# Kernel optimization log

Hardware: AMD Instinct MI355X
Metric: run time of the kernel (lower is better)

The kernel has to match this reference:

```python
import jax, jax.numpy as jnp
import numpy as np
from jax import lax

D_MODEL = 1024
D_STATE = 16
D_CONV = 4
EXPAND = 2
INNER = EXPAND * D_MODEL


def setup_inputs() -> dict:
    key = jax.random.key(0)
    ks = jax.random.split(key, 8)
    B, L = 2, 1024
    x = jax.random.normal(ks[0], (B, L, D_MODEL), dtype=jnp.float32)
    W_in = jax.random.normal(ks[1], (2 * INNER, D_MODEL), dtype=jnp.float32) * (1.0 / np.sqrt(D_MODEL))
    conv_w = jax.random.normal(ks[2], (INNER, 1, D_CONV), dtype=jnp.float32) * (1.0 / np.sqrt(D_CONV))
    conv_b = jax.random.normal(ks[3], (INNER,), dtype=jnp.float32) * 0.02
    A = jax.random.normal(ks[4], (INNER, D_STATE), dtype=jnp.float32) * 0.1
    B_param = jax.random.normal(ks[5], (INNER, D_STATE), dtype=jnp.float32) * 0.1
    C_param = jax.random.normal(ks[6], (INNER, D_STATE), dtype=jnp.float32) * 0.1
    D_param = jnp.ones((INNER,), dtype=jnp.float32)
    W_out = jax.random.normal(ks[7], (D_MODEL, INNER), dtype=jnp.float32) * (1.0 / np.sqrt(INNER))
    return {"x": x, "W_in": W_in, "conv_w": conv_w, "conv_b": conv_b,
            "A": A, "B_param": B_param, "C_param": C_param, "D_param": D_param,
            "W_out": W_out}


def _mamba_fwd(x, W_in, conv_w, conv_b, A, B_param, C_param, W_out):
    Bsz, L, _ = x.shape
    inner = A.shape[0]
    # in_proj then interleaved split: view (B,L,inner,2) -> x=[...,0], gate=[...,1]
    xp = jnp.einsum('bld,ed->ble', x, W_in).reshape(Bsz, L, inner, 2)
    u, gate = xp[..., 0], xp[..., 1]
    # depthwise causal conv (torch pads both sides d_conv-1 then slices [:L] == left pad only)
    u_ncl = jnp.transpose(u, (0, 2, 1))  # (B, inner, L)
    conv = lax.conv_general_dilated(
        u_ncl, conv_w,
        window_strides=(1,), padding=[(D_CONV - 1, 0)],
        dimension_numbers=('NCH', 'OIH', 'NCH'),
        feature_group_count=inner)
    conv = conv + conv_b[None, :, None]
    xc = jnp.transpose(conv, (0, 2, 1))  # (B, L, inner)
    delta = jax.nn.sigmoid(xc)
    # discretized params, time-major for scan: (L, B, inner, d_state)
    a = jnp.transpose(A[None, None] * delta[..., None], (1, 0, 2, 3))
    bx = jnp.transpose(B_param[None, None] * (delta * xc)[..., None], (1, 0, 2, 3))

    def step(state, inp):
        a_l, bx_l = inp
        state = a_l * state + bx_l                       # (B, inner, d_state)
        y = jnp.einsum('bns,ns->bn', state, C_param)     # (B, inner)
        return state, y

    state0 = jnp.zeros((Bsz, inner, A.shape[1]), dtype=x.dtype)
    _, ys = lax.scan(step, state0, (a, bx))              # ys: (L, B, inner)
    out = jnp.transpose(ys, (1, 0, 2)) * jax.nn.sigmoid(gate)
    return jnp.einsum('bln,dn->bld', out, W_out)


def reference(x, W_in, conv_w, conv_b, A, B_param, C_param, D_param, W_out):
    # D_param is defined by the module but unused in its forward; kept for fidelity.
    return _mamba_fwd(x, W_in, conv_w, conv_b, A, B_param, C_param, W_out)
```

## Files before the change

kernel.cpp:

```cpp
#include <hip/hip_runtime.h>
#include <hip/hip_bf16.h>

#define D_MODEL 1024
#define INNER   2048
#define NPROJ   4096
#define BSZ     2
#define LSEQ    1024
#define MROWS   (BSZ*LSEQ)

#define CHUNK 32
#define WARM  24
#define NCHK  (LSEQ / CHUNK)

using short8   = __attribute__((ext_vector_type(8))) short;
using ushort8  = __attribute__((ext_vector_type(8))) unsigned short;
using f32x4    = __attribute__((ext_vector_type(4))) float;
using i32x4    = __attribute__((ext_vector_type(4))) int;
using char16v  = __attribute__((ext_vector_type(16))) char;
typedef unsigned short ushort;
typedef unsigned char uchar;

#define MFMA16(A,B,Cv) __builtin_amdgcn_mfma_f32_16x16x32_bf16(A,B,Cv,0,0,0)
#define MFMAI8(A,B,Cv) __builtin_amdgcn_mfma_i32_16x16x64_i8(A,B,Cv,0,0,0)

__device__ __forceinline__ ushort tobf(float x) {
    return (ushort)(__builtin_bit_cast(unsigned, x) >> 16);
}
__device__ __forceinline__ float frombf(ushort h) {
    return __builtin_bit_cast(float, ((unsigned)h) << 16);
}
__device__ __forceinline__ void glds16(const void* g, void* l) {
    __builtin_amdgcn_global_load_lds((const __attribute__((address_space(1))) void*)g,
                                     (__attribute__((address_space(3))) void*)l, 16, 0, 0);
}

__global__ __launch_bounds__(256) void quant_rows(
    const float* __restrict__ W, uchar* __restrict__ Wh, uchar* __restrict__ Wl,
    float* __restrict__ sW, int RW,
    const float* __restrict__ X, uchar* __restrict__ Xh, uchar* __restrict__ Xl,
    float* __restrict__ sX)
{
    const int K = 1024, KT64 = K / 64;
    int gw = blockIdx.x * 4 + (threadIdx.x >> 6);
    int lane = threadIdx.x & 63;
    const float* src; uchar *dh, *dl; float* ss; int r;
    if (gw < RW) { r = gw;      src = W + (size_t)r * K; dh = Wh; dl = Wl; ss = sW; }
    else         { r = gw - RW; src = X + (size_t)r * K; dh = Xh; dl = Xl; ss = sX; }

    float v[16];
#pragma unroll
    for (int p = 0; p < 4; ++p) {
        float4 f = *reinterpret_cast<const float4*>(src + lane * 16 + p * 4);
        v[p*4+0] = f.x; v[p*4+1] = f.y; v[p*4+2] = f.z; v[p*4+3] = f.w;
    }
    float mx = 0.f;
#pragma unroll
    for (int j = 0; j < 16; ++j) mx = fmaxf(mx, fabsf(v[j]));
#pragma unroll
    for (int off = 1; off < 64; off <<= 1) mx = fmaxf(mx, __shfl_xor(mx, off));
    float s1 = fmaxf(mx, 1e-20f) / 127.f;
    if (lane == 0) ss[r] = s1;
    float inv = 1.f / s1;
    char16v hb, lb;
#pragma unroll
    for (int j = 0; j < 16; ++j) {
        float t = v[j] * inv;
        float h = rintf(t);
        float l = rintf((t - h) * 256.f);
        l = fminf(fmaxf(l, -128.f), 127.f);
        hb[j] = (char)(int)h;
        lb[j] = (char)(int)l;
    }
    size_t byte = (((size_t)(r >> 4) * KT64 + (lane >> 2)) * 64
                   + ((lane & 3) << 4) + (r & 15)) * 16;
    *reinterpret_cast<i32x4*>(dh + byte) = *reinterpret_cast<const i32x4*>(&hb);
    *reinterpret_cast<i32x4*>(dl + byte) = *reinterpret_cast<const i32x4*>(&lb);
}

__global__ __launch_bounds__(512, 1) void gemm1_i8(
    const uchar* __restrict__ Xh, const uchar* __restrict__ Xl, const float* __restrict__ sX,
    const uchar* __restrict__ Wh, const uchar* __restrict__ Wl, const float* __restrict__ sW,
    float* __restrict__ C)
{
    constexpr int KT64 = D_MODEL / 64;
    constexpr int NT = 16;
    __shared__ uchar Ah[3][8192], Al[3][8192];
    __shared__ uchar Bh[3][16384], Bl[3][16384];

    const int tid = threadIdx.x;
    const int wid = tid >> 6, lane = tid & 63;
    const int lm = lane & 15, lk = lane >> 4;

    constexpr int NTX = NPROJ / 256;
    constexpr int CPX = (NTX * (MROWS / 128)) / 8;
    int lin = blockIdx.y * NTX + blockIdx.x;
    int swz = (lin & 7) * CPX + (lin >> 3);
    const int m0 = (swz / NTX) * 128, n0 = (swz % NTX) * 256;
    const int wm = (wid >> 2) * 64, wn = (wid & 3) * 64;

    i32x4 acc1[4][4] = {};
    i32x4 acc2[4][4] = {};

    auto issueB = [&](const uchar* __restrict__ src, uchar* dst, int t, int ci) {
        int s = wid + ci * 8;
        const uchar* g = src + ((size_t)((n0 >> 4) + s) * KT64 + t) * 1024 + lane * 16;
        glds16(g, dst + s * 1024);
    };
    auto issueA = [&](const uchar* __restrict__ src, uchar* dst, int t) {
        const uchar* g = src + ((size_t)((m0 >> 4) + wid) * KT64 + t) * 1024 + lane * 16;
        glds16(g, dst + wid * 1024);
    };
    auto stageTile = [&](int t, int b) {
        issueB(Wh, &Bh[b][0], t, 0); issueB(Wh, &Bh[b][0], t, 1);
        issueB(Wl, &Bl[b][0], t, 0); issueB(Wl, &Bl[b][0], t, 1);
        issueA(Xh, &Ah[b][0], t);    issueA(Xl, &Al[b][0], t);
    };

    stageTile(0, 0);
    stageTile(1, 1);
    asm volatile("s_waitcnt vmcnt(6)" ::: "memory");
    __builtin_amdgcn_s_barrier();

    i32x4 ah[4], bh[4];
#pragma unroll
    for (int i = 0; i < 4; ++i)
        ah[i] = *reinterpret_cast<const i32x4*>(&Ah[0][((wm >> 4) + i) * 1024 + lane * 16]);
#pragma unroll
    for (int q = 0; q < 4; ++q)
        bh[q] = *reinterpret_cast<const i32x4*>(&Bh[0][((wn >> 4) + q) * 1024 + lane * 16]);

    int cur = 0;
    for (int t = 0; t < NT; ++t) {
        int nxt = cur + 1; if (nxt == 3) nxt = 0;
        int stg = cur + 2; if (stg >= 3) stg -= 3;
        const bool pf = (t + 2 < NT);
        i32x4 bl[4], al[4];

        asm volatile("s_waitcnt lgkmcnt(0)" ::: "memory");
        __builtin_amdgcn_sched_barrier(0);
        __builtin_amdgcn_s_setprio(1);
#pragma unroll
        for (int i = 0; i < 4; ++i)
#pragma unroll
            for (int q = 0; q < 4; ++q)
                acc1[i][q] = MFMAI8(ah[i], bh[q], acc1[i][q]);
        __builtin_amdgcn_s_setprio(0);
#pragma unroll
        for (int q = 0; q < 4; ++q)
            bl[q] = *reinterpret_cast<const i32x4*>(&Bl[cur][((wn >> 4) + q) * 1024 + lane * 16]);
        if (pf) {
            issueB(Wh, &Bh[stg][0], t + 2, 0);
            issueB(Wh, &Bh[stg][0], t + 2, 1);
        }

        asm volatile("s_waitcnt lgkmcnt(0)" ::: "memory");
        __builtin_amdgcn_sched_barrier(0);
        __builtin_amdgcn_s_setprio(1);
#pragma unroll
        for (int i = 0; i < 4; ++i)
#pragma unroll
            for (int q = 0; q < 4; ++q)
                acc2[i][q] = MFMAI8(ah[i], bl[q], acc2[i][q]);
        __builtin_amdgcn_s_setprio(0);
#pragma unroll
        for (int i = 0; i < 4; ++i)
            al[i] = *reinterpret_cast<const i32x4*>(&Al[cur][((wm >> 4) + i) * 1024 + lane * 16]);
        if (pf) {
            issueB(Wl, &Bl[stg][0], t + 2, 0);
            issueB(Wl, &Bl[stg][0], t + 2, 1);
        }
        __builtin_amdgcn_s_barrier();

        asm volatile("s_waitcnt lgkmcnt(0)" ::: "memory");
        __builtin_amdgcn_sched_barrier(0);
        __builtin_amdgcn_s_setprio(1);
#pragma unroll
        for (int i = 0; i < 4; ++i)
#pragma unroll
            for (int q = 0; q < 4; ++q)
                acc2[i][q] = MFMAI8(al[i], bh[q], acc2[i][q]);
        __builtin_amdgcn_s_setprio(0);
        if (pf) {
            issueA(Xh, &Ah[stg][0], t + 2);
            issueA(Xl, &Al[stg][0], t + 2);
        }
        if (pf) asm volatile("s_waitcnt vmcnt(6)" ::: "memory");
        else    asm volatile("s_waitcnt vmcnt(0)" ::: "memory");
        __builtin_amdgcn_s_barrier();

        if (t + 1 < NT) {
#pragma unroll
            for (int i = 0; i < 4; ++i)
                ah[i] = *reinterpret_cast<const i32x4*>(&Ah[nxt][((wm >> 4) + i) * 1024 + lane * 16]);
#pragma unroll
            for (int q = 0; q < 4; ++q)
                bh[q] = *reinterpret_cast<const i32x4*>(&Bh[nxt][((wn >> 4) + q) * 1024 + lane * 16]);
        }
        cur = nxt;
    }

#pragma unroll
    for (int i = 0; i < 4; ++i) {
        int r0 = m0 + wm + i * 16 + lk * 4;
        float4 s4 = *reinterpret_cast<const float4*>(&sX[r0]);
        float sa[4] = {s4.x, s4.y, s4.z, s4.w};
#pragma unroll
        for (int j = 0; j < 4; ++j) {
            int col = n0 + wn + j * 16 + lm;
            float sb = sW[col];
#pragma unroll
            for (int r = 0; r < 4; ++r) {
                float o = sa[r] * sb *
                    ((float)acc1[i][j][r] + (float)acc2[i][j][r] * 0.00390625f);
                C[(size_t)(r0 + r) * NPROJ + col] = o;
            }
        }
    }
}

template<int K>
__device__ __forceinline__ void split_chunk(const float* __restrict__ in,
                                            ushort* __restrict__ hi,
                                            ushort* __restrict__ lo, int c) {
    int l = c & 63, sub = c >> 6;
    constexpr int KT = K / 32;
    int kt = sub % KT, rt = sub / KT;
    const float* src = in + (size_t)(rt * 16 + (l & 15)) * K + kt * 32 + (l >> 4) * 8;
    ushort8 h, lw;
#pragma unroll
    for (int j = 0; j < 8; ++j) {
        float x = src[j];
        h[j]  = tobf(x);
        lw[j] = tobf(x - frombf(h[j]));
    }
    *reinterpret_cast<ushort8*>(&hi[(size_t)c * 8]) = h;
    *reinterpret_cast<ushort8*>(&lo[(size_t)c * 8]) = lw;
}

template<int K>
__global__ __launch_bounds__(256) void splitbf_frag(const float* __restrict__ in,
                                                    ushort* __restrict__ hi,
                                                    ushort* __restrict__ lo, int nchunks) {
    int c = blockIdx.x * 256 + threadIdx.x;
    if (c >= nchunks) return;
    split_chunk<K>(in, hi, lo, c);
}

template<int BN, int NCOL, int K, int SPLITK, bool PARTIAL, int NBUF, int NTHR>
__global__ __launch_bounds__(NTHR, 1) void gemm_pipe(
    const ushort* __restrict__ Agh, const ushort* __restrict__ Agl,
    const ushort* __restrict__ Bgh, const ushort* __restrict__ Bgl,
    float* __restrict__ C0, float* __restrict__ Crest)
{
    constexpr int BM = 128;
    constexpr int NW = NTHR / 64;
    constexpr int KT = K / 32;
    constexpr int NT = KT / SPLITK;
    constexpr int CB = (BN / 16) / NW;
    constexpr int CA = (BM / 16) / NW;
    __shared__ ushort Ah[NBUF][BM * 32], Al[NBUF][BM * 32];
    __shared__ ushort Bh[NBUF][BN * 32], Bl[NBUF][BN * 32];

    const int tid = threadIdx.x;
    const int wid = tid >> 6, lane = tid & 63;
    const int lm = lane & 15, lk = lane >> 4;

    constexpr int NTX = NCOL / BN;
    constexpr int NXY = NTX * (MROWS / BM);
    constexpr int CPX = NXY / 8;
    int lin = blockIdx.y * NTX + blockIdx.x;
    int swz = (lin & 7) * CPX + (lin >> 3);
    const int m0 = (swz / NTX) * BM, n0 = (swz % NTX) * BN;
    const int t0 = (SPLITK > 1 ? blockIdx.z : 0) * NT;
    const int wm = (NW == 8) ? (wid >> 2) * 64 : (wid >> 1) * 64;
    const int wn = (NW == 8) ? (wid & 3) * 64 : (wid & 1) * 64;

    f32x4 acc[4][4] = {};

    auto issueB = [&](const ushort* __restrict__ src, ushort* dst, int tg) {
#pragma unroll
        for (int ci = 0; ci < CB; ++ci) {
            int s = wid + ci * NW;
            const ushort* g = src + ((size_t)((n0 >> 4) + s) * KT + tg) * 512 + lane * 8;
            glds16(g, dst + s * 512);
        }
    };
    auto issueA = [&](const ushort* __restrict__ src, ushort* dst, int tg) {
#pragma unroll
        for (int ci = 0; ci < CA; ++ci) {
            int s = wid + ci * NW;
            const ushort* g = src + ((size_t)((m0 >> 4) + s) * KT + tg) * 512 + lane * 8;
            glds16(g, dst + s * 512);
        }
    };
    auto stageTile = [&](int t, int b) {
        issueB(Bgh, &Bh[b][0], t0 + t);
        issueB(Bgl, &Bl[b][0], t0 + t);
        issueA(Agh, &Ah[b][0], t0 + t);
        issueA(Agl, &Al[b][0], t0 + t);
    };

    if constexpr (NBUF == 3) {
        stageTile(0, 0);
        stageTile(1, 1);
        asm volatile("s_waitcnt vmcnt(6)" ::: "memory");
    } else {
        stageTile(0, 0);
        asm volatile("s_waitcnt vmcnt(0)" ::: "memory");
    }
    __builtin_amdgcn_s_barrier();

    short8 ah[4], bh[4];
#pragma unroll
    for (int i = 0; i < 4; ++i)
        ah[i] = *reinterpret_cast<const short8*>(&Ah[0][((wm >> 4) + i) * 512 + lane * 8]);
#pragma unroll
    for (int q = 0; q < 4; ++q)
        bh[q] = *reinterpret_cast<const short8*>(&Bh[0][((wn >> 4) + q) * 512 + lane * 8]);

    int cur = 0;
    for (int t = 0; t < NT; ++t) {
        int nxt, stg;
        bool pf;
        if constexpr (NBUF == 3) {
            nxt = cur + 1; if (nxt == 3) nxt = 0;
            stg = cur + 2; if (stg >= 3) stg -= 3;
            pf = (t + 2 < NT);
        } else {
            nxt = cur ^ 1;
            stg = nxt;
            pf = (t + 1 < NT);
        }
        const int tpre = (NBUF == 3) ? t + 2 : t + 1;
        short8 bl[4], al[4];

        asm volatile("s_waitcnt lgkmcnt(0)" ::: "memory");
        __builtin_amdgcn_sched_barrier(0);
        __builtin_amdgcn_s_setprio(1);
#pragma unroll
        for (int i = 0; i < 4; ++i)
#pragma unroll
            for (int q = 0; q < 4; ++q)
                acc[i][q] = MFMA16(ah[i], bh[q], acc[i][q]);
        __builtin_amdgcn_s_setprio(0);
#pragma unroll
        for (int q = 0; q < 4; ++q)
            bl[q] = *reinterpret_cast<const short8*>(&Bl[cur][((wn >> 4) + q) * 512 + lane * 8]);
        if (pf) issueB(Bgh, &Bh[stg][0], t0 + tpre);

        asm volatile("s_waitcnt lgkmcnt(0)" ::: "memory");
        __builtin_amdgcn_sched_barrier(0);
        __builtin_amdgcn_s_setprio(1);
#pragma unroll
        for (int i = 0; i < 4; ++i)
#pragma unroll
            for (int q = 0; q < 4; ++q)
                acc[i][q] = MFMA16(ah[i], bl[q], acc[i][q]);
        __builtin_amdgcn_s_setprio(0);
#pragma unroll
        for (int i = 0; i < 4; ++i)
            al[i] = *reinterpret_cast<const short8*>(&Al[cur][((wm >> 4) + i) * 512 + lane * 8]);
        if (pf) issueB(Bgl, &Bl[stg][0], t0 + tpre);
        __builtin_amdgcn_s_barrier();

        asm volatile("s_waitcnt lgkmcnt(0)" ::: "memory");
        __builtin_amdgcn_sched_barrier(0);
        __builtin_amdgcn_s_setprio(1);
#pragma unroll
        for (int i = 0; i < 4; ++i)
#pragma unroll
            for (int q = 0; q < 4; ++q)
                acc[i][q] = MFMA16(al[i], bh[q], acc[i][q]);
        __builtin_amdgcn_s_setprio(0);
        if (pf) {
            issueA(Agh, &Ah[stg][0], t0 + tpre);
            issueA(Agl, &Al[stg][0], t0 + tpre);
        }
        if (NBUF == 3 && pf) asm volatile("s_waitcnt vmcnt(6)" ::: "memory");
        else                 asm volatile("s_waitcnt vmcnt(0)" ::: "memory");
        __builtin_amdgcn_s_barrier();

        if (t + 1 < NT) {
#pragma unroll
            for (int i = 0; i < 4; ++i)
                ah[i] = *reinterpret_cast<const short8*>(&Ah[nxt][((wm >> 4) + i) * 512 + lane * 8]);
#pragma unroll
            for (int q = 0; q < 4; ++q)
                bh[q] = *reinterpret_cast<const short8*>(&Bh[nxt][((wn >> 4) + q) * 512 + lane * 8]);
        }
        cur = nxt;
    }

    float* C = C0;
    if constexpr (PARTIAL) {
        int kz = blockIdx.z;
        if (kz != 0) C = Crest + (size_t)(kz - 1) * MROWS * NCOL;
    }
#pragma unroll
    for (int i = 0; i < 4; ++i)
#pragma unroll
        for (int j = 0; j < 4; ++j)
#pragma unroll
            for (int r = 0; r < 4; ++r) {
                int row = m0 + wm + i * 16 + lk * 4 + r;
                int col = n0 + wn + j * 16 + lm;
                C[(size_t)row * NCOL + col] = acc[i][j][r];
            }
}

__global__ __launch_bounds__(256) void reduce_sk(float* __restrict__ out,
                                                 const float* __restrict__ rest) {
    constexpr size_t MN = (size_t)MROWS * D_MODEL;
    size_t i = ((size_t)blockIdx.x * 256 + threadIdx.x) * 4;
    f32x4 a = *reinterpret_cast<const f32x4*>(&out[i]);
    f32x4 b = *reinterpret_cast<const f32x4*>(&rest[i]);
    f32x4 c = *reinterpret_cast<const f32x4*>(&rest[MN + i]);
    f32x4 d = *reinterpret_cast<const f32x4*>(&rest[2 * MN + i]);
    *reinterpret_cast<f32x4*>(&out[i]) = (a + b) + (c + d);
}

__global__ __launch_bounds__(256) void scan_kernel(
    const float* __restrict__ xp,
    const float* __restrict__ conv_w, const float* __restrict__ conv_b,
    const float* __restrict__ Aa, const float* __restrict__ Bp, const float* __restrict__ Cp,
    ushort* __restrict__ yhi, ushort* __restrict__ ylo)
{
    const int NB = INNER / 256;
    int tid = threadIdx.x;
    int bi = blockIdx.x;
    int b  = bi / (NCHK * NB);
    int r  = bi % (NCHK * NB);
    int ch = r / NB;
    int n  = (r % NB) * 256 + tid;

    float4 w = *reinterpret_cast<const float4*>(&conv_w[n * 4]);
    float cb = conv_b[n];
    float An[16], Bn[16], Cn[16], st[16];
#pragma unroll
    for (int i = 0; i < 16; i += 4) {
        float4 va = *reinterpret_cast<const float4*>(&Aa[n * 16 + i]);
        float4 vb = *reinterpret_cast<const float4*>(&Bp[n * 16 + i]);
        float4 vc = *reinterpret_cast<const float4*>(&Cp[n * 16 + i]);
        An[i]=va.x; An[i+1]=va.y; An[i+2]=va.z; An[i+3]=va.w;
        Bn[i]=vb.x; Bn[i+1]=vb.y; Bn[i+2]=vb.z; Bn[i+3]=vb.w;
        Cn[i]=vc.x; Cn[i+1]=vc.y; Cn[i+2]=vc.z; Cn[i+3]=vc.w;
    }
#pragma unroll
    for (int s = 0; s < 16; ++s) st[s] = 0.f;

    int out0 = ch * CHUNK;
    int lstart = (out0 >= WARM) ? (out0 - WARM) : 0;
    float u0 = 0.f, u1 = 0.f, u2 = 0.f;
    const float* xb = xp + (size_t)b * LSEQ * NPROJ;
    size_t fcol = (size_t)(n >> 5) * 512 + ((n >> 3) & 3) * 128 + (n & 7);

    for (int l = lstart; l < out0; l += 8) {
        float uv[8];
#pragma unroll
        for (int i = 0; i < 8; ++i)
            uv[i] = xb[(size_t)(l + i) * NPROJ + 2 * n];
#pragma unroll
        for (int i = 0; i < 8; ++i) {
            float ul = uv[i];
            float xc = cb + w.x * u0 + w.y * u1 + w.z * u2 + w.w * ul;
            u0 = u1; u1 = u2; u2 = ul;
            float d = 1.f / (1.f + __expf(-xc));
            float dxc = d * xc;
#pragma unroll
            for (int s = 0; s < 16; ++s)
                st[s] = (An[s] * d) * st[s] + Bn[s] * dxc;
        }
    }
    for (int lt = 0; lt < CHUNK; lt += 8) {
        float uv[8], gv[8];
#pragma unroll
        for (int i = 0; i < 8; ++i) {
            float2 ug = *reinterpret_cast<const float2*>(
                &xb[(size_t)(out0 + lt + i) * NPROJ + 2 * n]);
            uv[i] = ug.x; gv[i] = ug.y;
        }
#pragma unroll
        for (int i = 0; i < 8; ++i) {
            float ul = uv[i];
            float xc = cb + w.x * u0 + w.y * u1 + w.z * u2 + w.w * ul;
            u0 = u1; u1 = u2; u2 = ul;
            float d = 1.f / (1.f + __expf(-xc));
            float dxc = d * xc;
            float y0 = 0.f, y1 = 0.f, y2 = 0.f, y3 = 0.f;
#pragma unroll
            for (int s = 0; s < 16; s += 4) {
                st[s + 0] = (An[s + 0] * d) * st[s + 0] + Bn[s + 0] * dxc;
                st[s + 1] = (An[s + 1] * d) * st[s + 1] + Bn[s + 1] * dxc;
                st[s + 2] = (An[s + 2] * d) * st[s + 2] + Bn[s + 2] * dxc;
                st[s + 3] = (An[s + 3] * d) * st[s + 3] + Bn[s + 3] * dxc;
                y0 += st[s + 0] * Cn[s + 0];
                y1 += st[s + 1] * Cn[s + 1];
                y2 += st[s + 2] * Cn[s + 2];
                y3 += st[s + 3] * Cn[s + 3];
            }
            float y = (y0 + y1) + (y2 + y3);
            float g = 1.f / (1.f + __expf(-gv[i]));
            float o = y * g;
            int R = b * LSEQ + out0 + lt + i;
            size_t fi = ((size_t)(R >> 4) * 64) * 512 + fcol + (R & 15) * 8;
            ushort hh = tobf(o);
            yhi[fi] = hh;
            ylo[fi] = tobf(o - frombf(hh));
        }
    }
}

extern "C" void kernel_launch(void* const* d_in, const int* in_sizes, int n_in,
                              void* d_out, int out_size, void* d_ws, size_t ws_size,
                              hipStream_t stream) {
    const float* x      = (const float*)d_in[0];
    const float* W_in   = (const float*)d_in[1];
    const float* conv_w = (const float*)d_in[2];
    const float* conv_b = (const float*)d_in[3];
    const float* A      = (const float*)d_in[4];
    const float* Bp     = (const float*)d_in[5];
    const float* Cp     = (const float*)d_in[6];
    const float* W_out  = (const float*)d_in[8];
    float* out = (float*)d_out;

    char* ws = (char*)d_ws;
    float* xp    = (float*)ws;
    uchar* Wh8   = (uchar*)(ws + (32u << 20));
    uchar* Wl8   = (uchar*)(ws + (36u << 20));
    float* sW    = (float*)(ws + (40u << 20));
    ushort* yghi = (ushort*)(ws + (32u << 20));
    ushort* yglo = (ushort*)(ws + (40u << 20));
    ushort* Wohi = (ushort*)ws;
    ushort* Wolo = (ushort*)(ws + (4u << 20));
    float*  Prest = (float*)(ws + (8u << 20));
    uchar* xh8 = (uchar*)d_out;
    uchar* xl8 = xh8 + (2u << 20);
    float* sX  = (float*)(xh8 + (4u << 20));

    dim3 blk(256);
    quant_rows<<<dim3((NPROJ + MROWS) / 4), blk, 0, stream>>>(
        W_in, Wh8, Wl8, sW, NPROJ, x, xh8, xl8, sX);
    gemm1_i8<<<dim3(16, 16), dim3(512), 0, stream>>>(
        xh8, xl8, sX, Wh8, Wl8, sW, xp);
    scan_kernel<<<dim3(BSZ * NCHK * (INNER / 256)), blk, 0, stream>>>(
        xp, conv_w, conv_b, A, Bp, Cp, yghi, yglo);
    splitbf_frag<INNER><<<dim3((D_MODEL * INNER / 8) / 256), blk, 0, stream>>>(
        W_out, Wohi, Wolo, D_MODEL * INNER / 8);
    gemm_pipe<128, D_MODEL, INNER, 4, true, 2, 256>
        <<<dim3(8, 16, 4), dim3(256), 0, stream>>>(yghi, yglo, Wohi, Wolo, out, Prest);
    reduce_sk<<<dim3((MROWS * D_MODEL / 4) / 256), blk, 0, stream>>>(out, Prest);
}
```

Baseline: 104.7 us.

## Switch output projection GEMM from split-bf16 to int8 hi/lo quantized MFMA

The output projection GEMM now uses the same int8 hi/lo per-row-scaled scheme as the input projection, running i8 MFMAs instead of bf16 MFMAs. The goal is to use the higher int8 matrix throughput for the compute-heavy out-proj GEMM. The scan kernel now writes plain fp32 gated outputs, and a generalized quantization kernel (templated on K) quantizes both those activations and W_out. The cost is an extra full fp32 round trip of the 2048x2048 activation buffer through memory. The approximation still depends on the two-level int8 split keeping enough precision.

```diff
diff --git a/kernel.cpp b/kernel.cpp
--- a/kernel.cpp
+++ b/kernel.cpp
@@ -12,69 +12,66 @@
 #define WARM  24
 #define NCHK  (LSEQ / CHUNK)
 
-using short8   = __attribute__((ext_vector_type(8))) short;
-using ushort8  = __attribute__((ext_vector_type(8))) unsigned short;
 using f32x4    = __attribute__((ext_vector_type(4))) float;
 using i32x4    = __attribute__((ext_vector_type(4))) int;
 using char16v  = __attribute__((ext_vector_type(16))) char;
 typedef unsigned short ushort;
 typedef unsigned char uchar;
 
-#define MFMA16(A,B,Cv) __builtin_amdgcn_mfma_f32_16x16x32_bf16(A,B,Cv,0,0,0)
 #define MFMAI8(A,B,Cv) __builtin_amdgcn_mfma_i32_16x16x64_i8(A,B,Cv,0,0,0)
 
-__device__ __forceinline__ ushort tobf(float x) {
-    return (ushort)(__builtin_bit_cast(unsigned, x) >> 16);
-}
-__device__ __forceinline__ float frombf(ushort h) {
-    return __builtin_bit_cast(float, ((unsigned)h) << 16);
-}
 __device__ __forceinline__ void glds16(const void* g, void* l) {
     __builtin_amdgcn_global_load_lds((const __attribute__((address_space(1))) void*)g,
                                      (__attribute__((address_space(3))) void*)l, 16, 0, 0);
 }
 
-__global__ __launch_bounds__(256) void quant_rows(
-    const float* __restrict__ W, uchar* __restrict__ Wh, uchar* __restrict__ Wl,
-    float* __restrict__ sW, int RW,
-    const float* __restrict__ X, uchar* __restrict__ Xh, uchar* __restrict__ Xl,
-    float* __restrict__ sX)
+template<int K>
+__global__ __launch_bounds__(256) void quant2src(
+    const float* __restrict__ S1, uchar* __restrict__ h1, uchar* __restrict__ l1,
+    float* __restrict__ sc1, int R1,
+    const float* __restrict__ S2, uchar* __restrict__ h2, uchar* __restrict__ l2,
+    float* __restrict__ sc2)
 {
-    const int K = 1024, KT64 = K / 64;
+    constexpr int CH = K / 1024;
+    constexpr int KT64 = K / 64;
     int gw = blockIdx.x * 4 + (threadIdx.x >> 6);
     int lane = threadIdx.x & 63;
     const float* src; uchar *dh, *dl; float* ss; int r;
-    if (gw < RW) { r = gw;      src = W + (size_t)r * K; dh = Wh; dl = Wl; ss = sW; }
-    else         { r = gw - RW; src = X + (size_t)r * K; dh = Xh; dl = Xl; ss = sX; }
-
-    float v[16];
-#pragma unroll
-    for (int p = 0; p < 4; ++p) {
-        float4 f = *reinterpret_cast<const float4*>(src + lane * 16 + p * 4);
+    if (gw < R1) { r = gw;      src = S1 + (size_t)r * K; dh = h1; dl = l1; ss = sc1; }
+    else         { r = gw - R1; src = S2 + (size_t)r * K; dh = h2; dl = l2; ss = sc2; }
+
+    float v[16 * CH];
+#pragma unroll
+    for (int p = 0; p < 4 * CH; ++p) {
+        float4 f = *reinterpret_cast<const float4*>(src + lane * 16 * CH + p * 4);
         v[p*4+0] = f.x; v[p*4+1] = f.y; v[p*4+2] = f.z; v[p*4+3] = f.w;
     }
     float mx = 0.f;
 #pragma unroll
-    for (int j = 0; j < 16; ++j) mx = fmaxf(mx, fabsf(v[j]));
+    for (int j = 0; j < 16 * CH; ++j) mx = fmaxf(mx, fabsf(v[j]));
 #pragma unroll
     for (int off = 1; off < 64; off <<= 1) mx = fmaxf(mx, __shfl_xor(mx, off));
     float s1 = fmaxf(mx, 1e-20f) / 127.f;
     if (lane == 0) ss[r] = s1;
     float inv = 1.f / s1;
-    char16v hb, lb;
-#pragma unroll
-    for (int j = 0; j < 16; ++j) {
-        float t = v[j] * inv;
-        float h = rintf(t);
-        float l = rintf((t - h) * 256.f);
-        l = fminf(fmaxf(l, -128.f), 127.f);
-        hb[j] = (char)(int)h;
-        lb[j] = (char)(int)l;
-    }
-    size_t byte = (((size_t)(r >> 4) * KT64 + (lane >> 2)) * 64
-                   + ((lane & 3) << 4) + (r & 15)) * 16;
-    *reinterpret_cast<i32x4*>(dh + byte) = *reinterpret_cast<const i32x4*>(&hb);
-    *reinterpret_cast<i32x4*>(dl + byte) = *reinterpret_cast<const i32x4*>(&lb);
+#pragma unroll
+    for (int c = 0; c < CH; ++c) {
+        char16v hb, lb;
+#pragma unroll
+        for (int j = 0; j < 16; ++j) {
+            float t = v[c * 16 + j] * inv;
+            float h = rintf(t);
+            float l = rintf((t - h) * 256.f);
+            l = fminf(fmaxf(l, -128.f), 127.f);
+            hb[j] = (char)(int)h;
+            lb[j] = (char)(int)l;
+        }
+        int gc = lane * CH + c;
+        size_t byte = (((size_t)(r >> 4) * KT64 + (gc >> 2)) * 64
+                       + ((gc & 3) << 4) + (r & 15)) * 16;
+        *reinterpret_cast<i32x4*>(dh + byte) = *reinterpret_cast<const i32x4*>(&hb);
+        *reinterpret_cast<i32x4*>(dl + byte) = *reinterpret_cast<const i32x4*>(&lb);
+    }
 }
 
 __global__ __launch_bounds__(512, 1) void gemm1_i8(
@@ -218,121 +215,72 @@
     }
 }
 
-template<int K>
-__device__ __forceinline__ void split_chunk(const float* __restrict__ in,
-                                            ushort* __restrict__ hi,
-                                            ushort* __restrict__ lo, int c) {
-    int l = c & 63, sub = c >> 6;
-    constexpr int KT = K / 32;
-    int kt = sub % KT, rt = sub / KT;
-    const float* src = in + (size_t)(rt * 16 + (l & 15)) * K + kt * 32 + (l >> 4) * 8;
-    ushort8 h, lw;
-#pragma unroll
-    for (int j = 0; j < 8; ++j) {
-        float x = src[j];
-        h[j]  = tobf(x);
-        lw[j] = tobf(x - frombf(h[j]));
-    }
-    *reinterpret_cast<ushort8*>(&hi[(size_t)c * 8]) = h;
-    *reinterpret_cast<ushort8*>(&lo[(size_t)c * 8]) = lw;
-}
-
-template<int K>
-__global__ __launch_bounds__(256) void splitbf_frag(const float* __restrict__ in,
-                                                    ushort* __restrict__ hi,
-                                                    ushort* __restrict__ lo, int nchunks) {
-    int c = blockIdx.x * 256 + threadIdx.x;
-    if (c >= nchunks) return;
-    split_chunk<K>(in, hi, lo, c);
-}
-
-template<int BN, int NCOL, int K, int SPLITK, bool PARTIAL, int NBUF, int NTHR>
-__global__ __launch_bounds__(NTHR, 1) void gemm_pipe(
-    const ushort* __restrict__ Agh, const ushort* __restrict__ Agl,
-    const ushort* __restrict__ Bgh, const ushort* __restrict__ Bgl,
+__global__ __launch_bounds__(256, 2) void gemm2_i8(
+    const uchar* __restrict__ Yh, const uchar* __restrict__ Yl, const float* __restrict__ sY,
+    const uchar* __restrict__ Wh, const uchar* __restrict__ Wl, const float* __restrict__ sW,
     float* __restrict__ C0, float* __restrict__ Crest)
 {
-    constexpr int BM = 128;
-    constexpr int NW = NTHR / 64;
-    constexpr int KT = K / 32;
-    constexpr int NT = KT / SPLITK;
-    constexpr int CB = (BN / 16) / NW;
-    constexpr int CA = (BM / 16) / NW;
-    __shared__ ushort Ah[NBUF][BM * 32], Al[NBUF][BM * 32];
-    __shared__ ushort Bh[NBUF][BN * 32], Bl[NBUF][BN * 32];
+    constexpr int KT64 = INNER / 64;
+    constexpr int SPLITK = 4;
+    constexpr int NT = KT64 / SPLITK;
+    __shared__ uchar Ah[2][8192], Al[2][8192];
+    __shared__ uchar Bh[2][8192], Bl[2][8192];
 
     const int tid = threadIdx.x;
     const int wid = tid >> 6, lane = tid & 63;
     const int lm = lane & 15, lk = lane >> 4;
 
-    constexpr int NTX = NCOL / BN;
-    constexpr int NXY = NTX * (MROWS / BM);
-    constexpr int CPX = NXY / 8;
+    constexpr int NTX = D_MODEL / 128;
+    constexpr int CPX = (NTX * (MROWS / 128)) / 8;
     int lin = blockIdx.y * NTX + blockIdx.x;
     int swz = (lin & 7) * CPX + (lin >> 3);
-    const int m0 = (swz / NTX) * BM, n0 = (swz % NTX) * BN;
-    const int t0 = (SPLITK > 1 ? blockIdx.z : 0) * NT;
-    const int wm = (NW == 8) ? (wid >> 2) * 64 : (wid >> 1) * 64;
-    const int wn = (NW == 8) ? (wid & 3) * 64 : (wid & 1) * 64;
-
-    f32x4 acc[4][4] = {};
-
-    auto issueB = [&](const ushort* __restrict__ src, ushort* dst, int tg) {
-#pragma unroll
-        for (int ci = 0; ci < CB; ++ci) {
-            int s = wid + ci * NW;
-            const ushort* g = src + ((size_t)((n0 >> 4) + s) * KT + tg) * 512 + lane * 8;
-            glds16(g, dst + s * 512);
+    const int m0 = (swz / NTX) * 128, n0 = (swz % NTX) * 128;
+    const int t0 = blockIdx.z * NT;
+    const int wm = (wid >> 1) * 64, wn = (wid & 1) * 64;
+
+    i32x4 acc1[4][4] = {};
+    i32x4 acc2[4][4] = {};
+
+    auto issueB = [&](const uchar* __restrict__ src, uchar* dst, int tg) {
+#pragma unroll
+        for (int ci = 0; ci < 2; ++ci) {
+            int s = wid + ci * 4;
+            const uchar* g = src + ((size_t)((n0 >> 4) + s) * KT64 + tg) * 1024 + lane * 16;
+            glds16(g, dst + s * 1024);
         }
     };
-    auto issueA = [&](const ushort* __restrict__ src, ushort* dst, int tg) {
-#pragma unroll
-        for (int ci = 0; ci < CA; ++ci) {
-            int s = wid + ci * NW;
-            const ushort* g = src + ((size_t)((m0 >> 4) + s) * KT + tg) * 512 + lane * 8;
-            glds16(g, dst + s * 512);
+    auto issueA = [&](const uchar* __restrict__ src, uchar* dst, int tg) {
+#pragma unroll
+        for (int ci = 0; ci < 2; ++ci) {
+            int s = wid + ci * 4;
+            const uchar* g = src + ((size_t)((m0 >> 4) + s) * KT64 + tg) * 1024 + lane * 16;
+            glds16(g, dst + s * 1024);
         }
     };
-    auto stageTile = [&](int t, int b) {
-        issueB(Bgh, &Bh[b][0], t0 + t);
-        issueB(Bgl, &Bl[b][0], t0 + t);
-        issueA(Agh, &Ah[b][0], t0 + t);
-        issueA(Agl, &Al[b][0], t0 + t);
+    auto stageTile = [&](int tg, int b) {
+        issueB(Wh, &Bh[b][0], tg);
+        issueB(Wl, &Bl[b][0], tg);
+        issueA(Yh, &Ah[b][0], tg);
+        issueA(Yl, &Al[b][0], tg);
     };
 
-    if constexpr (NBUF == 3) {
-        stageTile(0, 0);
-        stageTile(1, 1);
-        asm volatile("s_waitcnt vmcnt(6)" ::: "memory");
-    } else {
-        stageTile(0, 0);
-        asm volatile("s_waitcnt vmcnt(0)" ::: "memory");
-    }
+    stageTile(t0, 0);
+    asm volatile("s_waitcnt vmcnt(0)" ::: "memory");
     __builtin_amdgcn_s_barrier();
 
-    short8 ah[4], bh[4];
+    i32x4 ah[4], bh[4];
 #pragma unroll
     for (int i = 0; i < 4; ++i)
-        ah[i] = *reinterpret_cast<const short8*>(&Ah[0][((wm >> 4) + i) * 512 + lane * 8]);
+        ah[i] = *reinterpret_cast<const i32x4*>(&Ah[0][((wm >> 4) + i) * 1024 + lane * 16]);
 #pragma unroll
     for (int q = 0; q < 4; ++q)
-        bh[q] = *reinterpret_cast<const short8*>(&Bh[0][((wn >> 4) + q) * 512 + lane * 8]);
+        bh[q] = *reinterpret_cast<const i32x4*>(&Bh[0][((wn >> 4) + q) * 1024 + lane * 16]);
 
     int cur = 0;
     for (int t = 0; t < NT; ++t) {
-        int nxt, stg;
-        bool pf;
-        if constexpr (NBUF == 3) {
-            nxt = cur + 1; if (nxt == 3) nxt = 0;
-            stg = cur + 2; if (stg >= 3) stg -= 3;
-            pf = (t + 2 < NT);
-        } else {
-            nxt = cur ^ 1;
-            stg = nxt;
-            pf = (t + 1 < NT);
-        }
-        const int tpre = (NBUF == 3) ? t + 2 : t + 1;
-        short8 bl[4], al[4];
+        int nxt = cur ^ 1;
+        const bool pf = (t + 1 < NT);
+        i32x4 bl[4], al[4];
 
         asm volatile("s_waitcnt lgkmcnt(0)" ::: "memory");
         __builtin_amdgcn_sched_barrier(0);
@@ -341,12 +289,12 @@
         for (int i = 0; i < 4; ++i)
 #pragma unroll
             for (int q = 0; q < 4; ++q)
-                acc[i][q] = MFMA16(ah[i], bh[q], acc[i][q]);
+                acc1[i][q] = MFMAI8(ah[i], bh[q], acc1[i][q]);
         __builtin_amdgcn_s_setprio(0);
 #pragma unroll
         for (int q = 0; q < 4; ++q)
-            bl[q] = *reinterpret_cast<const short8*>(&Bl[cur][((wn >> 4) + q) * 512 + lane * 8]);
-        if (pf) issueB(Bgh, &Bh[stg][0], t0 + tpre);
+            bl[q] = *reinterpret_cast<const i32x4*>(&Bl[cur][((wn >> 4) + q) * 1024 + lane * 16]);
+        if (pf) issueB(Wh, &Bh[nxt][0], t0 + t + 1);
 
         asm volatile("s_waitcnt lgkmcnt(0)" ::: "memory");
         __builtin_amdgcn_sched_barrier(0);
@@ -355,12 +303,12 @@
         for (int i = 0; i < 4; ++i)
 #pragma unroll
             for (int q = 0; q < 4; ++q)
-                acc[i][q] = MFMA16(ah[i], bl[q], acc[i][q]);
+                acc2[i][q] = MFMAI8(ah[i], bl[q], acc2[i][q]);
         __builtin_amdgcn_s_setprio(0);
 #pragma unroll
         for (int i = 0; i < 4; ++i)
-            al[i] = *reinterpret_cast<const short8*>(&Al[cur][((wm >> 4) + i) * 512 + lane * 8]);
-        if (pf) issueB(Bgl, &Bl[stg][0], t0 + tpre);
+            al[i] = *reinterpret_cast<const i32x4*>(&Al[cur][((wm >> 4) + i) * 1024 + lane * 16]);
+        if (pf) issueB(Wl, &Bl[nxt][0], t0 + t + 1);
         __builtin_amdgcn_s_barrier();
 
         asm volatile("s_waitcnt lgkmcnt(0)" ::: "memory");
@@ -370,42 +318,45 @@
         for (int i = 0; i < 4; ++i)
 #pragma unroll
             for (int q = 0; q < 4; ++q)
-                acc[i][q] = MFMA16(al[i], bh[q], acc[i][q]);
+                acc2[i][q] = MFMAI8(al[i], bh[q], acc2[i][q]);
         __builtin_amdgcn_s_setprio(0);
         if (pf) {
-            issueA(Agh, &Ah[stg][0], t0 + tpre);
-            issueA(Agl, &Al[stg][0], t0 + tpre);
-        }
-        if (NBUF == 3 && pf) asm volatile("s_waitcnt vmcnt(6)" ::: "memory");
-        else                 asm volatile("s_waitcnt vmcnt(0)" ::: "memory");
+            issueA(Yh, &Ah[nxt][0], t0 + t + 1);
+            issueA(Yl, &Al[nxt][0], t0 + t + 1);
+        }
+        asm volatile("s_waitcnt vmcnt(0)" ::: "memory");
         __builtin_amdgcn_s_barrier();
 
         if (t + 1 < NT) {
 #pragma unroll
             for (int i = 0; i < 4; ++i)
-                ah[i] = *reinterpret_cast<const short8*>(&Ah[nxt][((wm >> 4) + i) * 512 + lane * 8]);
-#pragma unroll
-            for (int q = 0; q < 4; ++q)
-                bh[q] = *reinterpret_cast<const short8*>(&Bh[nxt][((wn >> 4) + q) * 512 + lane * 8]);
+                ah[i] = *reinterpret_cast<const i32x4*>(&Ah[nxt][((wm >> 4) + i) * 1024 + lane * 16]);
+#pragma unroll
+            for (int q = 0; q < 4; ++q)
+                bh[q] = *reinterpret_cast<const i32x4*>(&Bh[nxt][((wn >> 4) + q) * 1024 + lane * 16]);
         }
         cur = nxt;
     }
 
-    float* C = C0;
-    if constexpr (PARTIAL) {
-        int kz = blockIdx.z;
-        if (kz != 0) C = Crest + (size_t)(kz - 1) * MROWS * NCOL;
-    }
-#pragma unroll
-    for (int i = 0; i < 4; ++i)
-#pragma unroll
-        for (int j = 0; j < 4; ++j)
+    int kz = blockIdx.z;
+    float* C = (kz == 0) ? C0 : (Crest + (size_t)(kz - 1) * MROWS * D_MODEL);
+#pragma unroll
+    for (int i = 0; i < 4; ++i) {
+        int r0 = m0 + wm + i * 16 + lk * 4;
+        float4 s4 = *reinterpret_cast<const float4*>(&sY[r0]);
+        float sa[4] = {s4.x, s4.y, s4.z, s4.w};
+#pragma unroll
+        for (int j = 0; j < 4; ++j) {
+            int col = n0 + wn + j * 16 + lm;
+            float sb = sW[col];
 #pragma unroll
             for (int r = 0; r < 4; ++r) {
-                int row = m0 + wm + i * 16 + lk * 4 + r;
-                int col = n0 + wn + j * 16 + lm;
-                C[(size_t)row * NCOL + col] = acc[i][j][r];
+                float o = sa[r] * sb *
+                    ((float)acc1[i][j][r] + (float)acc2[i][j][r] * 0.00390625f);
+                C[(size_t)(r0 + r) * D_MODEL + col] = o;
             }
+        }
+    }
 }
 
 __global__ __launch_bounds__(256) void reduce_sk(float* __restrict__ out,
@@ -423,7 +374,7 @@
     const float* __restrict__ xp,
     const float* __restrict__ conv_w, const float* __restrict__ conv_b,
     const float* __restrict__ Aa, const float* __restrict__ Bp, const float* __restrict__ Cp,
-    ushort* __restrict__ yhi, ushort* __restrict__ ylo)
+    float* __restrict__ yg)
 {
     const int NB = INNER / 256;
     int tid = threadIdx.x;
@@ -452,7 +403,6 @@
     int lstart = (out0 >= WARM) ? (out0 - WARM) : 0;
     float u0 = 0.f, u1 = 0.f, u2 = 0.f;
     const float* xb = xp + (size_t)b * LSEQ * NPROJ;
-    size_t fcol = (size_t)(n >> 5) * 512 + ((n >> 3) & 3) * 128 + (n & 7);
 
     for (int l = lstart; l < out0; l += 8) {
         float uv[8];
@@ -500,12 +450,8 @@
             }
             float y = (y0 + y1) + (y2 + y3);
             float g = 1.f / (1.f + __expf(-gv[i]));
-            float o = y * g;
             int R = b * LSEQ + out0 + lt + i;
-            size_t fi = ((size_t)(R >> 4) * 64) * 512 + fcol + (R & 15) * 8;
-            ushort hh = tobf(o);
-            yhi[fi] = hh;
-            ylo[fi] = tobf(o - frombf(hh));
+            yg[(size_t)R * INNER + n] = y * g;
         }
     }
 }
@@ -528,25 +474,28 @@
     uchar* Wh8   = (uchar*)(ws + (32u << 20));
     uchar* Wl8   = (uchar*)(ws + (36u << 20));
     float* sW    = (float*)(ws + (40u << 20));
-    ushort* yghi = (ushort*)(ws + (32u << 20));
-    ushort* yglo = (ushort*)(ws + (40u << 20));
-    ushort* Wohi = (ushort*)ws;
-    ushort* Wolo = (ushort*)(ws + (4u << 20));
-    float*  Prest = (float*)(ws + (8u << 20));
+    float* yg    = (float*)(ws + (32u << 20));
+    uchar* ygh8  = (uchar*)ws;
+    uchar* ygl8  = (uchar*)(ws + (4u << 20));
+    float* Prest = (float*)(ws + (8u << 20));
+    uchar* woh8  = (uchar*)(ws + (48u << 20));
+    uchar* wol8  = (uchar*)(ws + (50u << 20));
+    float* sY    = (float*)(ws + (52u << 20));
+    float* sWo   = (float*)(ws + (52u << 20) + (16u << 10));
     uchar* xh8 = (uchar*)d_out;
     uchar* xl8 = xh8 + (2u << 20);
     float* sX  = (float*)(xh8 + (4u << 20));
 
     dim3 blk(256);
-    quant_rows<<<dim3((NPROJ + MROWS) / 4), blk, 0, stream>>>(
+    quant2src<D_MODEL><<<dim3((NPROJ + MROWS) / 4), blk, 0, stream>>>(
         W_in, Wh8, Wl8, sW, NPROJ, x, xh8, xl8, sX);
     gemm1_i8<<<dim3(16, 16), dim3(512), 0, stream>>>(
         xh8, xl8, sX, Wh8, Wl8, sW, xp);
     scan_kernel<<<dim3(BSZ * NCHK * (INNER / 256)), blk, 0, stream>>>(
-        xp, conv_w, conv_b, A, Bp, Cp, yghi, yglo);
-    splitbf_frag<INNER><<<dim3((D_MODEL * INNER / 8) / 256), blk, 0, stream>>>(
-        W_out, Wohi, Wolo, D_MODEL * INNER / 8);
-    gemm_pipe<128, D_MODEL, INNER, 4, true, 2, 256>
-        <<<dim3(8, 16, 4), dim3(256), 0, stream>>>(yghi, yglo, Wohi, Wolo, out, Prest);
+        xp, conv_w, conv_b, A, Bp, Cp, yg);
+    quant2src<INNER><<<dim3((MROWS + D_MODEL) / 4), blk, 0, stream>>>(
+        yg, ygh8, ygl8, sY, MROWS, W_out, woh8, wol8, sWo);
+    gemm2_i8<<<dim3(8, 16, 4), blk, 0, stream>>>(
+        ygh8, ygl8, sY, woh8, wol8, sWo, out, Prest);
     reduce_sk<<<dim3((MROWS * D_MODEL / 4) / 256), blk, 0, stream>>>(out, Prest);
 }
```

New measurement: 100.1 us. 4.3% less time.
